# Kernel tuning notes

Hardware: AMD Instinct MI355X
Metric: run time of the kernel (lower is better)

## Reference

```python
import jax, jax.numpy as jnp
import numpy as np

N_NODES = 100000
N_EDGES = 1600000
N_GRAPHS = 64
F_IN = 256
HID = 256
PROJ = 128
L = 4


def setup_inputs() -> dict:
    key = jax.random.key(0)
    ks = jax.random.split(key, 12)
    x = jax.random.normal(ks[0], (N_NODES, F_IN), dtype=jnp.float32)
    edge_index = jax.random.randint(ks[1], (2, N_EDGES), 0, N_NODES)
    batch = jnp.sort(jax.random.randint(ks[2], (N_NODES,), 0, N_GRAPHS))
    s = 0.05
    # SAGEConv per layer: lin_l (applied to mean-aggregated neighbors, with bias)
    # and lin_r (applied to root node, no bias). All layers are 256->256, stacked.
    Wl = jax.random.normal(ks[3], (L, HID, HID), dtype=jnp.float32) * s
    bl = jax.random.normal(ks[4], (L, HID), dtype=jnp.float32) * s
    Wr = jax.random.normal(ks[5], (L, HID, HID), dtype=jnp.float32) * s
    gamma = jnp.ones((L, HID), dtype=jnp.float32)
    beta = jnp.zeros((L, HID), dtype=jnp.float32)
    W1 = jax.random.normal(ks[6], (HID, HID), dtype=jnp.float32) * s
    b1 = jnp.zeros((HID,), dtype=jnp.float32)
    W2 = jax.random.normal(ks[7], (HID, PROJ), dtype=jnp.float32) * s
    b2 = jnp.zeros((PROJ,), dtype=jnp.float32)
    return {"x": x, "edge_index": edge_index, "batch": batch,
            "Wl": Wl, "bl": bl, "Wr": Wr, "gamma": gamma, "beta": beta,
            "W1": W1, "b1": b1, "W2": W2, "b2": b2}


def _segment_mean(vals, seg_ids, num_segments):
    sums = jax.ops.segment_sum(vals, seg_ids, num_segments=num_segments)
    cnt = jax.ops.segment_sum(jnp.ones((vals.shape[0],), vals.dtype), seg_ids,
                              num_segments=num_segments)
    return sums / jnp.maximum(cnt, 1.0)[:, None]


def reference(x, edge_index, batch, Wl, bl, Wr, gamma, beta, W1, b1, W2, b2):
    src, dst = edge_index[0], edge_index[1]
    eps = 1e-5
    h = x
    for i in range(L):
        # SAGEConv: mean-aggregate neighbor features, then lin_l(aggr) + lin_r(root)
        aggr = _segment_mean(h[src], dst, N_NODES)          # [N, HID]
        h = aggr @ Wl[i] + bl[i] + h @ Wr[i]
        # BatchNorm1d (training-mode batch statistics, biased variance)
        mu = jnp.mean(h, axis=0)
        var = jnp.mean(jnp.square(h - mu), axis=0)
        h = (h - mu) * jax.lax.rsqrt(var + eps) * gamma[i] + beta[i]
        h = jax.nn.relu(h)
        # dropout omitted (inference / deterministic reference)
    g = _segment_mean(h, batch, N_GRAPHS)                   # [G, HID]
    z = jax.nn.relu(g @ W1 + b1) @ W2 + b2                  # [G, PROJ]
    # F.normalize(z, dim=1): L2 normalize with eps clamp
    norm = jnp.maximum(jnp.linalg.norm(z, axis=1, keepdims=True), 1e-12)
    return z / norm
```

## Files before the change

kernel.cpp:

```cpp
#include <hip/hip_runtime.h>

#define N_NODES 100000
#define M_PAD   100096
#define N_MBLK  782
#define N_EDGES 1600000
#define N_GRAPHS 64
#define HID 256
#define PROJ 128
#define NLAYERS 4

#define EBUF_STRIDE 8192
#define N_BUCKETS ((N_NODES + 255) / 256)
#define CSR_BLK 1024
#define EPT 10
#define CSR_NBLK ((N_EDGES + CSR_BLK * EPT - 1) / (CSR_BLK * EPT))
#define SENT 0xFFFFFFFFu
#define GEMM_BUF 24576

typedef unsigned short u16;
typedef unsigned long long u64;
typedef __attribute__((ext_vector_type(4))) float f32x4;
typedef __attribute__((ext_vector_type(2))) float vf2;

__device__ __forceinline__ u16 f2b(float f) {
  unsigned u = __float_as_uint(f);
  u = (u + 0x7FFF + ((u >> 16) & 1)) >> 16;
  return (u16)u;
}
__device__ __forceinline__ void gload16(const void* g, void* l) {
  __builtin_amdgcn_global_load_lds((const __attribute__((address_space(1))) void*)g,
                                   (__attribute__((address_space(3))) void*)l, 16, 0, 0);
}
__device__ __forceinline__ unsigned pack_fp8x4(float a, float b, float c, float d) {
  int v = __builtin_amdgcn_cvt_pk_fp8_f32(a, b, 0, false);
  v = __builtin_amdgcn_cvt_pk_fp8_f32(c, d, v, true);
  return (unsigned)v;
}
__device__ __forceinline__ unsigned char f2f8(float a) {
  return (unsigned char)(__builtin_amdgcn_cvt_pk_fp8_f32(a, a, 0, false) & 0xFF);
}
__device__ __forceinline__ void accf8(float* a, unsigned w) {
  vf2 lo = __builtin_amdgcn_cvt_pk_f32_fp8((int)w, false);
  vf2 hi = __builtin_amdgcn_cvt_pk_f32_fp8((int)w, true);
  a[0] += lo.x; a[1] += lo.y; a[2] += hi.x; a[3] += hi.y;
}
__device__ __forceinline__ void decf8(float* f, unsigned w) {
  vf2 lo = __builtin_amdgcn_cvt_pk_f32_fp8((int)w, false);
  vf2 hi = __builtin_amdgcn_cvt_pk_f32_fp8((int)w, true);
  f[0] = lo.x; f[1] = lo.y; f[2] = hi.x; f[3] = hi.y;
}

__global__ __launch_bounds__(1024) void bucket_scatter(
    const int* __restrict__ src, const int* __restrict__ dst,
    u64* __restrict__ bfill64, uint2* __restrict__ ebuf) {
  __shared__ int lhist[N_BUCKETS];
  __shared__ int lbase[N_BUCKETS];
  int t = threadIdx.x;
  int e0 = blockIdx.x * (CSR_BLK * EPT) + t;
  for (int i = t; i < N_BUCKETS; i += CSR_BLK) lhist[i] = 0;
  __syncthreads();
  int sv[EPT], dv[EPT];
#pragma unroll
  for (int j = 0; j < EPT; j++) {
    int e = e0 + j * CSR_BLK;
    if (e < N_EDGES) {
      sv[j] = src[e];
      dv[j] = dst[e];
      atomicAdd(&lhist[dv[j] >> 8], 1);
    } else {
      dv[j] = -1;
      sv[j] = 0;
    }
  }
  __syncthreads();
  for (int i = t; i < N_BUCKETS; i += CSR_BLK) {
    int c = lhist[i];
    if (c > 0) {
      int rounded = (c + 7) & ~7;
      u64 old = atomicAdd(&bfill64[(size_t)i * 8],
                          ((u64)rounded << 32) | (u64)c);
      int base = (int)(old >> 32);
      lbase[i] = base;
      for (int k = c; k < rounded; k++) {
        int p = base + k;
        if (p < EBUF_STRIDE) {
          uint2 q; q.x = 0; q.y = SENT;
          ebuf[(size_t)i * EBUF_STRIDE + p] = q;
        }
      }
      lhist[i] = 0;
    }
  }
  __syncthreads();
#pragma unroll
  for (int j = 0; j < EPT; j++) {
    if (dv[j] >= 0) {
      int b = dv[j] >> 8;
      int p = lbase[b] + atomicAdd(&lhist[b], 1);
      if (p < EBUF_STRIDE) {
        uint2 q;
        q.x = (unsigned)sv[j];
        q.y = (unsigned)dv[j];
        ebuf[(size_t)b * EBUF_STRIDE + p] = q;
      }
    }
  }
}

__global__ __launch_bounds__(512) void bucket_prefix(
    const u64* __restrict__ bfill64, int* __restrict__ bucket_base,
    int* __restrict__ row_ptr) {
  __shared__ int tile[512];
  int t = threadIdx.x;
  int v = 0;
  if (t < N_BUCKETS) {
    u64 w = bfill64[(size_t)t * 8];
    v = (int)(w & 0xFFFFFFFFull);
    if ((int)(w >> 32) > EBUF_STRIDE) v = min(v, EBUF_STRIDE);
  }
  tile[t] = v;
  __syncthreads();
  for (int off = 1; off < 512; off <<= 1) {
    int add = (t >= off) ? tile[t - off] : 0;
    __syncthreads();
    tile[t] += add;
    __syncthreads();
  }
  if (t < N_BUCKETS) bucket_base[t] = tile[t] - v;
  if (t == N_BUCKETS - 1) row_ptr[N_NODES] = tile[t];
}

__global__ __launch_bounds__(1024) void csr_build(
    const uint2* __restrict__ ebuf, const u64* __restrict__ bfill64,
    const int* __restrict__ bucket_base, int* __restrict__ row_ptr,
    float* __restrict__ inv_cnt, int* __restrict__ col) {
  __shared__ int hist[256];
  __shared__ int nscan[256];
  __shared__ int cursor[256];
  int b = blockIdx.x;
  int t = threadIdx.x;
  int nalloc = min((int)(bfill64[(size_t)b * 8] >> 32), EBUF_STRIDE);
  int bbase = bucket_base[b];
  if (t < 256) hist[t] = 0;
  __syncthreads();
  uint2 q[8];
#pragma unroll
  for (int k = 0; k < 8; k++) {
    int i = t + k * CSR_BLK;
    q[k].x = 0; q[k].y = SENT;
    if (i < nalloc) {
      q[k] = ebuf[(size_t)b * EBUF_STRIDE + i];
      if (q[k].y != SENT) atomicAdd(&hist[q[k].y & 255], 1);
    }
  }
  __syncthreads();
  if (t < 256) nscan[t] = hist[t];
  __syncthreads();
  for (int off = 1; off < 256; off <<= 1) {
    int add = 0;
    if (t < 256 && t >= off) add = nscan[t - off];
    __syncthreads();
    if (t < 256) nscan[t] += add;
    __syncthreads();
  }
  int nb = min(256, N_NODES - b * 256);
  if (t < 256) {
    int excl = nscan[t] - hist[t];
    cursor[t] = excl;
    if (t < nb) {
      row_ptr[b * 256 + t] = bbase + excl;
      inv_cnt[b * 256 + t] = 1.0f / fmaxf((float)hist[t], 1.0f);
    }
  }
  __syncthreads();
#pragma unroll
  for (int k = 0; k < 8; k++) {
    if (q[k].y != SENT) {
      int l = (int)(q[k].y & 255);
      int pos = bbase + atomicAdd(&cursor[l], 1);
      col[pos] = (int)q[k].x;
    }
  }
}

__global__ __launch_bounds__(256) void convert_x8(const float4* __restrict__ x,
                                                  unsigned* __restrict__ h8) {
  int i = blockIdx.x * blockDim.x + threadIdx.x;
  float4 v = x[i];
  h8[i] = pack_fp8x4(v.x, v.y, v.z, v.w);
}

__global__ __launch_bounds__(256) void convert_w8(const float* __restrict__ Wl,
                                                  const float* __restrict__ Wr,
                                                  unsigned* __restrict__ Wt8) {
  int idx = blockIdx.x * blockDim.x + threadIdx.x;
  int l = idx >> 15;
  int r = idx & 32767;
  int n = r >> 7;
  int k4 = (r & 127) * 4;
  float v[4];
#pragma unroll
  for (int j = 0; j < 4; j++) {
    int k = k4 + j;
    v[j] = (k < 256) ? Wl[(size_t)l * 65536 + k * 256 + n]
                     : Wr[(size_t)l * 65536 + (k - 256) * 256 + n];
  }
  Wt8[idx] = pack_fp8x4(v[0], v[1], v[2], v[3]);
}

__global__ __launch_bounds__(256) void aggregate_fp8(
    const unsigned char* __restrict__ h8, const int* __restrict__ row_ptr,
    const int* __restrict__ col, const float* __restrict__ inv_cnt,
    unsigned char* __restrict__ aggr8) {
  int node = blockIdx.x * 4 + (threadIdx.x >> 6);
  int lane = threadIdx.x & 63;
  int half = lane >> 5, l32 = lane & 31;
  int r0 = row_ptr[node], r1 = row_ptr[node + 1];
  float a[8] = {0.f, 0.f, 0.f, 0.f, 0.f, 0.f, 0.f, 0.f};
  int e = r0 + half;
  for (; e + 14 < r1; e += 16) {
    int s[8];
#pragma unroll
    for (int j = 0; j < 8; j++) s[j] = col[e + 2 * j];
    uint2 v[8];
#pragma unroll
    for (int j = 0; j < 8; j++)
      v[j] = *((const uint2*)(h8 + (size_t)s[j] * HID) + l32);
#pragma unroll
    for (int j = 0; j < 8; j++) { accf8(a, v[j].x); accf8(a + 4, v[j].y); }
  }
  for (; e + 6 < r1; e += 8) {
    int s0 = col[e], s1 = col[e + 2], s2 = col[e + 4], s3 = col[e + 6];
    uint2 v0 = *((const uint2*)(h8 + (size_t)s0 * HID) + l32);
    uint2 v1 = *((const uint2*)(h8 + (size_t)s1 * HID) + l32);
    uint2 v2 = *((const uint2*)(h8 + (size_t)s2 * HID) + l32);
    uint2 v3 = *((const uint2*)(h8 + (size_t)s3 * HID) + l32);
    accf8(a, v0.x); accf8(a + 4, v0.y);
    accf8(a, v1.x); accf8(a + 4, v1.y);
    accf8(a, v2.x); accf8(a + 4, v2.y);
    accf8(a, v3.x); accf8(a + 4, v3.y);
  }
  for (; e < r1; e += 2) {
    int s0 = col[e];
    uint2 v0 = *((const uint2*)(h8 + (size_t)s0 * HID) + l32);
    accf8(a, v0.x); accf8(a + 4, v0.y);
  }
#pragma unroll
  for (int j = 0; j < 8; j++) a[j] += __shfl_xor(a[j], 32, 64);
  if (half == 0) {
    float inv = inv_cnt[node];
    uint2 o;
    o.x = pack_fp8x4(a[0] * inv, a[1] * inv, a[2] * inv, a[3] * inv);
    o.y = pack_fp8x4(a[4] * inv, a[5] * inv, a[6] * inv, a[7] * inv);
    *((uint2*)(aggr8 + (size_t)node * HID) + l32) = o;
  }
}

__global__ __launch_bounds__(256, 2) void gemm_fused_fp8(
    const unsigned char* __restrict__ a8, const unsigned char* __restrict__ h8,
    const unsigned char* __restrict__ Bt8, unsigned char* __restrict__ hpre8,
    float* __restrict__ psum) {
  __shared__ unsigned char smem[2 * GEMM_BUF];
  __shared__ float bns[4][8][16][2];

  int tid = threadIdx.x;
  int wid = tid >> 6, lane = tid & 63;
  int m0 = blockIdx.x * 128;
  int q = lane >> 4, c = lane & 15;
  int wm = (wid >> 1) * 64, wn = (wid & 1) * 128;

  f32x4 zero = {0.f, 0.f, 0.f, 0.f};
  f32x4 acc[4][8];
#pragma unroll
  for (int mi = 0; mi < 4; mi++)
#pragma unroll
    for (int ni = 0; ni < 8; ni++) acc[mi][ni] = zero;

  int srowA0 = wid * 32 + (lane >> 2);
  int cgA0 = (lane & 3) ^ ((srowA0 >> 1) & 3);
  int srowA1 = srowA0 + 16;
  int cgA1 = (lane & 3) ^ ((srowA1 >> 1) & 3);
  int srowB[4], cgB[4];
#pragma unroll
  for (int j = 0; j < 4; j++) {
    srowB[j] = j * 64 + wid * 16 + (lane >> 2);
    cgB[j] = (lane & 3) ^ ((srowB[j] >> 1) & 3);
  }

  int aoff[4][2], boff[8][2];
#pragma unroll
  for (int mi = 0; mi < 4; mi++) {
    int row = wm + mi * 16 + c;
    int x = (row >> 1) & 3;
#pragma unroll
    for (int kk = 0; kk < 2; kk++) {
      int chunk = kk * 2 + (q >> 1);
      aoff[mi][kk] = row * 64 + ((chunk ^ x) << 4) + ((q & 1) << 3);
    }
  }
#pragma unroll
  for (int ni = 0; ni < 8; ni++) {
    int row = wn + ni * 16 + c;
    int x = (row >> 1) & 3;
#pragma unroll
    for (int kk = 0; kk < 2; kk++) {
      int chunk = kk * 2 + (q >> 1);
      boff[ni][kk] = row * 64 + ((chunk ^ x) << 4) + ((q & 1) << 3);
    }
  }

  auto stage = [&](int k0, int b) {
    const unsigned char* Asrc = (k0 < 256) ? a8 : h8;
    int ksrc = k0 & 255;
    unsigned char* As = smem + b * GEMM_BUF;
    unsigned char* Bs = As + 128 * 64;
    gload16(Asrc + ((size_t)(m0 + srowA0) * HID + ksrc + cgA0 * 16),
            &As[(wid * 32) * 64]);
    gload16(Asrc + ((size_t)(m0 + srowA1) * HID + ksrc + cgA1 * 16),
            &As[(wid * 32 + 16) * 64]);
#pragma unroll
    for (int j = 0; j < 4; j++)
      gload16(Bt8 + ((size_t)srowB[j] * 512 + k0 + cgB[j] * 16),
              &Bs[(j * 64 + wid * 16) * 64]);
  };

  stage(0, 0);
  __syncthreads();
#pragma unroll
  for (int t = 0; t < 8; ++t) {
    int cur = t & 1;
    if (t < 7) stage((t + 1) * 64, cur ^ 1);
    const unsigned char* As = smem + cur * GEMM_BUF;
    const unsigned char* Bs = As + 128 * 64;
    long long af[4][2], bfr[8][2];
#pragma unroll
    for (int mi = 0; mi < 4; mi++) {
      af[mi][0] = *(const long long*)&As[aoff[mi][0]];
      af[mi][1] = *(const long long*)&As[aoff[mi][1]];
    }
#pragma unroll
    for (int ni = 0; ni < 8; ni++) {
      bfr[ni][0] = *(const long long*)&Bs[boff[ni][0]];
      bfr[ni][1] = *(const long long*)&Bs[boff[ni][1]];
    }
#pragma unroll
    for (int mi = 0; mi < 4; mi++)
#pragma unroll
      for (int ni = 0; ni < 8; ni++) {
        acc[mi][ni] = __builtin_amdgcn_mfma_f32_16x16x32_fp8_fp8(
            af[mi][0], bfr[ni][0], acc[mi][ni], 0, 0, 0);
        acc[mi][ni] = __builtin_amdgcn_mfma_f32_16x16x32_fp8_fp8(
            af[mi][1], bfr[ni][1], acc[mi][ni], 0, 0, 0);
      }
    __syncthreads();
  }

  unsigned char* ep8 = smem;
  int rh = wid >> 1;
#pragma unroll
  for (int mi = 0; mi < 4; mi++) {
#pragma unroll
    for (int r = 0; r < 4; r++) {
      int r16 = q * 4 + r;
#pragma unroll
      for (int ni = 0; ni < 8; ni++)
        ep8[(rh * 16 + r16) * 256 + wn + ni * 16 + c] = f2f8(acc[mi][ni][r]);
    }
    __syncthreads();
    int u = tid;
#pragma unroll
    for (int j = 0; j < 2; j++, u += 256) {
      int lr = u >> 4;
      int cu = u & 15;
      int gm = m0 + (lr >> 4) * 64 + mi * 16 + (lr & 15);
      if (gm < N_NODES)
        ((uint4*)(hpre8 + (size_t)gm * HID))[cu] = ((const uint4*)ep8)[u];
    }
    __syncthreads();
  }

#pragma unroll
  for (int ni = 0; ni < 8; ni++) {
    float s = 0.f, s2 = 0.f;
#pragma unroll
    for (int mi = 0; mi < 4; mi++) {
#pragma unroll
      for (int r = 0; r < 4; r++) {
        int gm = m0 + wm + mi * 16 + q * 4 + r;
        float v = (gm < N_NODES) ? acc[mi][ni][r] : 0.f;
        s += v;
        s2 += v * v;
      }
    }
    s += __shfl_xor(s, 16, 64);
    s += __shfl_xor(s, 32, 64);
    s2 += __shfl_xor(s2, 16, 64);
    s2 += __shfl_xor(s2, 32, 64);
    if (q == 0) {
      bns[wid][ni][c][0] = s;
      bns[wid][ni][c][1] = s2;
    }
  }
  __syncthreads();
  {
    int wnh = tid >> 7, ni = (tid >> 4) & 7, cc = tid & 15;
    float s = bns[wnh][ni][cc][0] + bns[wnh + 2][ni][cc][0];
    float s2 = bns[wnh][ni][cc][1] + bns[wnh + 2][ni][cc][1];
    int coln = wnh * 128 + ni * 16 + cc;
    psum[(size_t)blockIdx.x * 512 + coln] = s;
    psum[(size_t)blockIdx.x * 512 + 256 + coln] = s2;
  }
}

#define BN_MID 16
__global__ __launch_bounds__(256) void bn_mid(const float* __restrict__ psum,
                                              float* __restrict__ tmp) {
  int b = blockIdx.x;
  int f = threadIdx.x;
  int mb0 = b * 49;
  int mb1 = min(mb0 + 49, N_MBLK);
  float s = 0.f, s2 = 0.f;
  for (int mb = mb0; mb < mb1; mb++) {
    s += psum[(size_t)mb * 512 + f];
    s2 += psum[(size_t)mb * 512 + 256 + f];
  }
  tmp[(size_t)b * 512 + f] = s;
  tmp[(size_t)b * 512 + 256 + f] = s2;
}

__global__ void bn_fin(const float* __restrict__ tmp,
                       const float* __restrict__ gamma,
                       const float* __restrict__ beta,
                       float* __restrict__ ss) {
  int f = threadIdx.x;
  float sum = 0.f, sq = 0.f;
#pragma unroll
  for (int b = 0; b < BN_MID; b++) {
    sum += tmp[(size_t)b * 512 + f];
    sq += tmp[(size_t)b * 512 + 256 + f];
  }
  const float invN = 1.0f / (float)N_NODES;
  float mu = sum * invN;
  float ex2 = sq * invN;
  float var = fmaxf(ex2 - mu * mu, 0.f);
  float sc = gamma[f] * rsqrtf(var + 1e-5f);
  ss[f] = sc;
  ss[HID + f] = beta[f] - mu * sc;
}

__global__ __launch_bounds__(256) void bn_apply_h8(const uint2* __restrict__ hpre8,
                                                   const float* __restrict__ ss,
                                                   uint2* __restrict__ h8out) {
  int idx0 = blockIdx.x * blockDim.x + threadIdx.x;
  int cb = (idx0 & 31) * 8;
  float sc[8], sh[8];
#pragma unroll
  for (int j = 0; j < 8; j++) { sc[j] = ss[cb + j]; sh[j] = ss[HID + cb + j]; }
  const int total = N_NODES * 32;
  const int step = gridDim.x * blockDim.x;
  for (int i = idx0; i < total; i += step) {
    uint2 v = hpre8[i];
    float f[8];
    decf8(f, v.x);
    decf8(f + 4, v.y);
#pragma unroll
    for (int j = 0; j < 8; j++)
      f[j] = fmaxf(fmaf(f[j], sc[j], sh[j]), 0.f);
    uint2 o;
    o.x = pack_fp8x4(f[0], f[1], f[2], f[3]);
    o.y = pack_fp8x4(f[4], f[5], f[6], f[7]);
    h8out[i] = o;
  }
}

__global__ __launch_bounds__(256) void pool_partial(
    const unsigned char* __restrict__ hpre8, const float* __restrict__ ss,
    const int* __restrict__ batch, float* __restrict__ partial) {
  __shared__ float red[256][9];
  int g = blockIdx.x;
  int i = blockIdx.y;
  int t = threadIdx.x;
  int a = 0, b = N_NODES;
  while (a < b) { int m = (a + b) >> 1; if (batch[m] < g) a = m + 1; else b = m; }
  int lo = a;
  b = N_NODES;
  while (a < b) { int m = (a + b) >> 1; if (batch[m] < g + 1) a = m + 1; else b = m; }
  int hi = a;
  int len = hi - lo;
  int clen = (len + 7) >> 3;
  int c0 = lo + i * clen;
  int c1 = min(c0 + clen, hi);

  int rs = t >> 5, cu = t & 31;
  int cb = cu * 8;
  float scv[8], shv[8];
#pragma unroll
  for (int j = 0; j < 8; j++) { scv[j] = ss[cb + j]; shv[j] = ss[HID + cb + j]; }
  float acc[8] = {0.f, 0.f, 0.f, 0.f, 0.f, 0.f, 0.f, 0.f};
  for (int r = c0 + rs; r < c1; r += 8) {
    uint2 v = *((const uint2*)(hpre8 + (size_t)r * HID) + cu);
    float f[8];
    decf8(f, v.x);
    decf8(f + 4, v.y);
#pragma unroll
    for (int j = 0; j < 8; j++)
      acc[j] += fmaxf(fmaf(f[j], scv[j], shv[j]), 0.f);
  }
#pragma unroll
  for (int j = 0; j < 8; j++) red[t][j] = acc[j];
  __syncthreads();
  int cc = t >> 3, j = t & 7;
  float sum = 0.f;
#pragma unroll
  for (int k = 0; k < 8; k++) sum += red[k * 32 + cc][j];
  partial[((size_t)g * 8 + i) * 256 + t] = sum;
}

__global__ __launch_bounds__(256) void pool_mlp_final(
    const float* __restrict__ partial, const int* __restrict__ batch,
    const float* __restrict__ W1, const float* __restrict__ b1,
    const float* __restrict__ W2, const float* __restrict__ b2,
    float* __restrict__ out) {
  __shared__ float gs[HID];
  __shared__ float ts[HID];
  __shared__ float rn[PROJ];
  int g = blockIdx.x;
  int t = threadIdx.x;
  int a = 0, b = N_NODES;
  while (a < b) { int m = (a + b) >> 1; if (batch[m] < g) a = m + 1; else b = m; }
  int lo = a;
  b = N_NODES;
  while (a < b) { int m = (a + b) >> 1; if (batch[m] < g + 1) a = m + 1; else b = m; }
  int len = a - lo;

  float sum = 0.f;
#pragma unroll
  for (int i = 0; i < 8; i++) sum += partial[((size_t)g * 8 + i) * 256 + t];
  float inv = 1.0f / fmaxf((float)len, 1.0f);
  gs[t] = sum * inv;
  __syncthreads();

  float s = b1[t];
  for (int k = 0; k < HID; k++) s = fmaf(gs[k], W1[(size_t)k * HID + t], s);
  ts[t] = fmaxf(s, 0.f);
  __syncthreads();
  float z = 0.f;
  if (t < PROJ) {
    z = b2[t];
    for (int k = 0; k < HID; k++) z = fmaf(ts[k], W2[(size_t)k * PROJ + t], z);
    rn[t] = z * z;
  }
  __syncthreads();
  for (int off = PROJ / 2; off > 0; off >>= 1) {
    if (t < off) rn[t] += rn[t + off];
    __syncthreads();
  }
  float norm = fmaxf(sqrtf(rn[0]), 1e-12f);
  if (t < PROJ) out[(size_t)g * PROJ + t] = z / norm;
}

extern "C" void kernel_launch(void* const* d_in, const int* in_sizes, int n_in,
                              void* d_out, int out_size, void* d_ws, size_t ws_size,
                              hipStream_t stream) {
  const float* x = (const float*)d_in[0];
  const int* ei = (const int*)d_in[1];
  const int* src = ei;
  const int* dst = ei + N_EDGES;
  const int* batch = (const int*)d_in[2];
  const float* Wl = (const float*)d_in[3];
  const float* Wr = (const float*)d_in[5];
  const float* gamma = (const float*)d_in[6];
  const float* beta = (const float*)d_in[7];
  const float* W1 = (const float*)d_in[8];
  const float* b1 = (const float*)d_in[9];
  const float* W2 = (const float*)d_in[10];
  const float* b2 = (const float*)d_in[11];
  float* out = (float*)d_out;

  char* p = (char*)d_ws;
  const size_t H8 = (size_t)M_PAD * HID;
  unsigned char* hpre8 = (unsigned char*)p; p += H8;
  unsigned char* aggr8 = (unsigned char*)p; p += H8;
  unsigned char* h8 = (unsigned char*)p;    p += H8;
  unsigned char* Wt8 = (unsigned char*)p;   p += (size_t)NLAYERS * 512 * HID;
  int* col = (int*)p;    p += (size_t)N_EDGES * sizeof(int);
  int* row_ptr = (int*)p; p += 400016;
  float* inv_cnt = (float*)p; p += (size_t)N_NODES * sizeof(float);
  float* psum = (float*)p;    p += (size_t)N_MBLK * 512 * sizeof(float);
  float* tmp = (float*)p;     p += (size_t)BN_MID * 512 * sizeof(float);
  float* ss = (float*)p;      p += 512 * sizeof(float);
  float* partial = (float*)p; p += (size_t)N_GRAPHS * 8 * 256 * sizeof(float);
  uint2* ebuf = (uint2*)p;    p += (size_t)N_BUCKETS * EBUF_STRIDE * sizeof(uint2);

  u64* bfill64 = (u64*)hpre8;
  int* bucket_base = (int*)(bfill64 + (size_t)N_BUCKETS * 8);

  hipMemsetAsync(bfill64, 0, (size_t)N_BUCKETS * 8 * sizeof(u64), stream);
  bucket_scatter<<<CSR_NBLK, CSR_BLK, 0, stream>>>(src, dst, bfill64, ebuf);
  bucket_prefix<<<1, 512, 0, stream>>>(bfill64, bucket_base, row_ptr);
  csr_build<<<N_BUCKETS, CSR_BLK, 0, stream>>>(ebuf, bfill64, bucket_base,
                                               row_ptr, inv_cnt, col);

  convert_x8<<<N_NODES / 4, 256, 0, stream>>>((const float4*)x, (unsigned*)h8);
  convert_w8<<<(NLAYERS * 512 * HID / 4) / 256, 256, 0, stream>>>(Wl, Wr,
                                                                  (unsigned*)Wt8);

  for (int l = 0; l < NLAYERS; l++) {
    aggregate_fp8<<<N_NODES / 4, 256, 0, stream>>>(h8, row_ptr, col, inv_cnt, aggr8);
    gemm_fused_fp8<<<N_MBLK, 256, 0, stream>>>(aggr8, h8,
                                               Wt8 + (size_t)l * 512 * HID,
                                               hpre8, psum);
    bn_mid<<<BN_MID, 256, 0, stream>>>(psum, tmp);
    bn_fin<<<1, 256, 0, stream>>>(tmp, gamma + (size_t)l * HID,
                                  beta + (size_t)l * HID, ss);
    if (l < NLAYERS - 1) {
      bn_apply_h8<<<2048, 256, 0, stream>>>((const uint2*)hpre8, ss, (uint2*)h8);
    }
  }

  pool_partial<<<dim3(N_GRAPHS, 8), 256, 0, stream>>>(hpre8, ss, batch, partial);
  pool_mlp_final<<<N_GRAPHS, 256, 0, stream>>>(partial, batch, W1, b1, W2, b2, out);
}
```

Before: 770.8 us.

## Fuse neighbor mean-aggregation into the SAGE GEMM kernel via LDS

Result: slower. 1.204 ms (+56.2%).

```diff
diff --git a/kernel.cpp b/kernel.cpp
--- a/kernel.cpp
+++ b/kernel.cpp
@@ -15,18 +15,12 @@
 #define EPT 10
 #define CSR_NBLK ((N_EDGES + CSR_BLK * EPT - 1) / (CSR_BLK * EPT))
 #define SENT 0xFFFFFFFFu
-#define GEMM_BUF 24576
 
 typedef unsigned short u16;
 typedef unsigned long long u64;
 typedef __attribute__((ext_vector_type(4))) float f32x4;
 typedef __attribute__((ext_vector_type(2))) float vf2;
 
-__device__ __forceinline__ u16 f2b(float f) {
-  unsigned u = __float_as_uint(f);
-  u = (u + 0x7FFF + ((u >> 16) & 1)) >> 16;
-  return (u16)u;
-}
 __device__ __forceinline__ void gload16(const void* g, void* l) {
   __builtin_amdgcn_global_load_lds((const __attribute__((address_space(1))) void*)g,
                                    (__attribute__((address_space(3))) void*)l, 16, 0, 0);
@@ -208,60 +202,12 @@
   Wt8[idx] = pack_fp8x4(v[0], v[1], v[2], v[3]);
 }
 
-__global__ __launch_bounds__(256) void aggregate_fp8(
+__global__ __launch_bounds__(256, 2) void agg_gemm_fused(
     const unsigned char* __restrict__ h8, const int* __restrict__ row_ptr,
     const int* __restrict__ col, const float* __restrict__ inv_cnt,
-    unsigned char* __restrict__ aggr8) {
-  int node = blockIdx.x * 4 + (threadIdx.x >> 6);
-  int lane = threadIdx.x & 63;
-  int half = lane >> 5, l32 = lane & 31;
-  int r0 = row_ptr[node], r1 = row_ptr[node + 1];
-  float a[8] = {0.f, 0.f, 0.f, 0.f, 0.f, 0.f, 0.f, 0.f};
-  int e = r0 + half;
-  for (; e + 14 < r1; e += 16) {
-    int s[8];
-#pragma unroll
-    for (int j = 0; j < 8; j++) s[j] = col[e + 2 * j];
-    uint2 v[8];
-#pragma unroll
-    for (int j = 0; j < 8; j++)
-      v[j] = *((const uint2*)(h8 + (size_t)s[j] * HID) + l32);
-#pragma unroll
-    for (int j = 0; j < 8; j++) { accf8(a, v[j].x); accf8(a + 4, v[j].y); }
-  }
-  for (; e + 6 < r1; e += 8) {
-    int s0 = col[e], s1 = col[e + 2], s2 = col[e + 4], s3 = col[e + 6];
-    uint2 v0 = *((const uint2*)(h8 + (size_t)s0 * HID) + l32);
-    uint2 v1 = *((const uint2*)(h8 + (size_t)s1 * HID) + l32);
-    uint2 v2 = *((const uint2*)(h8 + (size_t)s2 * HID) + l32);
-    uint2 v3 = *((const uint2*)(h8 + (size_t)s3 * HID) + l32);
-    accf8(a, v0.x); accf8(a + 4, v0.y);
-    accf8(a, v1.x); accf8(a + 4, v1.y);
-    accf8(a, v2.x); accf8(a + 4, v2.y);
-    accf8(a, v3.x); accf8(a + 4, v3.y);
-  }
-  for (; e < r1; e += 2) {
-    int s0 = col[e];
-    uint2 v0 = *((const uint2*)(h8 + (size_t)s0 * HID) + l32);
-    accf8(a, v0.x); accf8(a + 4, v0.y);
-  }
-#pragma unroll
-  for (int j = 0; j < 8; j++) a[j] += __shfl_xor(a[j], 32, 64);
-  if (half == 0) {
-    float inv = inv_cnt[node];
-    uint2 o;
-    o.x = pack_fp8x4(a[0] * inv, a[1] * inv, a[2] * inv, a[3] * inv);
-    o.y = pack_fp8x4(a[4] * inv, a[5] * inv, a[6] * inv, a[7] * inv);
-    *((uint2*)(aggr8 + (size_t)node * HID) + l32) = o;
-  }
-}
-
-__global__ __launch_bounds__(256, 2) void gemm_fused_fp8(
-    const unsigned char* __restrict__ a8, const unsigned char* __restrict__ h8,
     const unsigned char* __restrict__ Bt8, unsigned char* __restrict__ hpre8,
     float* __restrict__ psum) {
-  __shared__ unsigned char smem[2 * GEMM_BUF];
-  __shared__ float bns[4][8][16][2];
+  __shared__ unsigned char smem[65536];
 
   int tid = threadIdx.x;
   int wid = tid >> 6, lane = tid & 63;
@@ -309,53 +255,155 @@
     }
   }
 
-  auto stage = [&](int k0, int b) {
-    const unsigned char* Asrc = (k0 < 256) ? a8 : h8;
-    int ksrc = k0 & 255;
-    unsigned char* As = smem + b * GEMM_BUF;
-    unsigned char* Bs = As + 128 * 64;
-    gload16(Asrc + ((size_t)(m0 + srowA0) * HID + ksrc + cgA0 * 16),
-            &As[(wid * 32) * 64]);
-    gload16(Asrc + ((size_t)(m0 + srowA1) * HID + ksrc + cgA1 * 16),
-            &As[(wid * 32 + 16) * 64]);
+  {
+    auto stageA = [&](int k0, int b) {
+      unsigned char* As = smem + b * 24576;
+      unsigned char* Bs = As + 8192;
+      int ksrc = k0 - 256;
+      gload16(h8 + ((size_t)(m0 + srowA0) * HID + ksrc + cgA0 * 16),
+              &As[(wid * 32) * 64]);
+      gload16(h8 + ((size_t)(m0 + srowA1) * HID + ksrc + cgA1 * 16),
+              &As[(wid * 32 + 16) * 64]);
+#pragma unroll
+      for (int j = 0; j < 4; j++)
+        gload16(Bt8 + ((size_t)srowB[j] * 512 + k0 + cgB[j] * 16),
+                &Bs[(j * 64 + wid * 16) * 64]);
+    };
+    stageA(256, 0);
+    __syncthreads();
+#pragma unroll
+    for (int t = 0; t < 4; ++t) {
+      int cur = t & 1;
+      if (t < 3) stageA(256 + (t + 1) * 64, cur ^ 1);
+      const unsigned char* As = smem + cur * 24576;
+      const unsigned char* Bs = As + 8192;
+      long long af[4][2], bfr[8][2];
+#pragma unroll
+      for (int mi = 0; mi < 4; mi++) {
+        af[mi][0] = *(const long long*)&As[aoff[mi][0]];
+        af[mi][1] = *(const long long*)&As[aoff[mi][1]];
+      }
+#pragma unroll
+      for (int ni = 0; ni < 8; ni++) {
+        bfr[ni][0] = *(const long long*)&Bs[boff[ni][0]];
+        bfr[ni][1] = *(const long long*)&Bs[boff[ni][1]];
+      }
+#pragma unroll
+      for (int mi = 0; mi < 4; mi++)
+#pragma unroll
+        for (int ni = 0; ni < 8; ni++) {
+          acc[mi][ni] = __builtin_amdgcn_mfma_f32_16x16x32_fp8_fp8(
+              af[mi][0], bfr[ni][0], acc[mi][ni], 0, 0, 0);
+          acc[mi][ni] = __builtin_amdgcn_mfma_f32_16x16x32_fp8_fp8(
+              af[mi][1], bfr[ni][1], acc[mi][ni], 0, 0, 0);
+        }
+      __syncthreads();
+    }
+  }
+
+  {
+    unsigned char* Bs = smem + 32768;
 #pragma unroll
     for (int j = 0; j < 4; j++)
-      gload16(Bt8 + ((size_t)srowB[j] * 512 + k0 + cgB[j] * 16),
+      gload16(Bt8 + ((size_t)srowB[j] * 512 + 0 + cgB[j] * 16),
               &Bs[(j * 64 + wid * 16) * 64]);
-  };
-
-  stage(0, 0);
-  __syncthreads();
-#pragma unroll
-  for (int t = 0; t < 8; ++t) {
-    int cur = t & 1;
-    if (t < 7) stage((t + 1) * 64, cur ^ 1);
-    const unsigned char* As = smem + cur * GEMM_BUF;
-    const unsigned char* Bs = As + 128 * 64;
-    long long af[4][2], bfr[8][2];
-#pragma unroll
-    for (int mi = 0; mi < 4; mi++) {
-      af[mi][0] = *(const long long*)&As[aoff[mi][0]];
-      af[mi][1] = *(const long long*)&As[aoff[mi][1]];
-    }
-#pragma unroll
-    for (int ni = 0; ni < 8; ni++) {
-      bfr[ni][0] = *(const long long*)&Bs[boff[ni][0]];
-      bfr[ni][1] = *(const long long*)&Bs[boff[ni][1]];
-    }
-#pragma unroll
-    for (int mi = 0; mi < 4; mi++)
+  }
+
+  {
+    int half = lane >> 5, l32 = lane & 31;
+    int kstep = l32 >> 3;
+    int chunk = (l32 >> 1) & 3;
+    int bytein = (l32 & 1) * 8;
+    for (int nloc = 0; nloc < 32; ++nloc) {
+      int row = wid * 32 + nloc;
+      int node = m0 + row;
+      float a[8] = {0.f, 0.f, 0.f, 0.f, 0.f, 0.f, 0.f, 0.f};
+      bool valid = (node < N_NODES);
+      if (valid) {
+        int r0 = row_ptr[node], r1 = row_ptr[node + 1];
+        int e = r0 + half;
+        for (; e + 14 < r1; e += 16) {
+          int s[8];
+#pragma unroll
+          for (int j = 0; j < 8; j++) s[j] = col[e + 2 * j];
+          uint2 v[8];
+#pragma unroll
+          for (int j = 0; j < 8; j++)
+            v[j] = *((const uint2*)(h8 + (size_t)s[j] * HID) + l32);
+#pragma unroll
+          for (int j = 0; j < 8; j++) { accf8(a, v[j].x); accf8(a + 4, v[j].y); }
+        }
+        for (; e + 6 < r1; e += 8) {
+          int s0 = col[e], s1 = col[e + 2], s2 = col[e + 4], s3 = col[e + 6];
+          uint2 v0 = *((const uint2*)(h8 + (size_t)s0 * HID) + l32);
+          uint2 v1 = *((const uint2*)(h8 + (size_t)s1 * HID) + l32);
+          uint2 v2 = *((const uint2*)(h8 + (size_t)s2 * HID) + l32);
+          uint2 v3 = *((const uint2*)(h8 + (size_t)s3 * HID) + l32);
+          accf8(a, v0.x); accf8(a + 4, v0.y);
+          accf8(a, v1.x); accf8(a + 4, v1.y);
+          accf8(a, v2.x); accf8(a + 4, v2.y);
+          accf8(a, v3.x); accf8(a + 4, v3.y);
+        }
+        for (; e < r1; e += 2) {
+          int s0 = col[e];
+          uint2 v0 = *((const uint2*)(h8 + (size_t)s0 * HID) + l32);
+          accf8(a, v0.x); accf8(a + 4, v0.y);
+        }
+      }
+#pragma unroll
+      for (int j = 0; j < 8; j++) a[j] += __shfl_xor(a[j], 32, 64);
+      if (half == 0) {
+        float inv = valid ? inv_cnt[node] : 0.f;
+        uint2 o;
+        o.x = pack_fp8x4(a[0] * inv, a[1] * inv, a[2] * inv, a[3] * inv);
+        o.y = pack_fp8x4(a[4] * inv, a[5] * inv, a[6] * inv, a[7] * inv);
+        int chx = chunk ^ ((row >> 1) & 3);
+        *(uint2*)(smem + kstep * 8192 + row * 64 + chx * 16 + bytein) = o;
+      }
+    }
+  }
+  __syncthreads();
+
+  {
+    auto stageBC = [&](int k0, int b) {
+      unsigned char* Bs = smem + 32768 + b * 16384;
+#pragma unroll
+      for (int j = 0; j < 4; j++)
+        gload16(Bt8 + ((size_t)srowB[j] * 512 + k0 + cgB[j] * 16),
+                &Bs[(j * 64 + wid * 16) * 64]);
+    };
+#pragma unroll
+    for (int t = 0; t < 4; ++t) {
+      int cur = t & 1;
+      if (t < 3) stageBC((t + 1) * 64, cur ^ 1);
+      const unsigned char* As = smem + t * 8192;
+      const unsigned char* Bs = smem + 32768 + cur * 16384;
+      long long af[4][2], bfr[8][2];
+#pragma unroll
+      for (int mi = 0; mi < 4; mi++) {
+        af[mi][0] = *(const long long*)&As[aoff[mi][0]];
+        af[mi][1] = *(const long long*)&As[aoff[mi][1]];
+      }
 #pragma unroll
       for (int ni = 0; ni < 8; ni++) {
-        acc[mi][ni] = __builtin_amdgcn_mfma_f32_16x16x32_fp8_fp8(
-            af[mi][0], bfr[ni][0], acc[mi][ni], 0, 0, 0);
-        acc[mi][ni] = __builtin_amdgcn_mfma_f32_16x16x32_fp8_fp8(
-            af[mi][1], bfr[ni][1], acc[mi][ni], 0, 0, 0);
-      }
-    __syncthreads();
-  }
-
-  unsigned char* ep8 = smem;
+        bfr[ni][0] = *(const long long*)&Bs[boff[ni][0]];
+        bfr[ni][1] = *(const long long*)&Bs[boff[ni][1]];
+      }
+#pragma unroll
+      for (int mi = 0; mi < 4; mi++)
+#pragma unroll
+        for (int ni = 0; ni < 8; ni++) {
+          acc[mi][ni] = __builtin_amdgcn_mfma_f32_16x16x32_fp8_fp8(
+              af[mi][0], bfr[ni][0], acc[mi][ni], 0, 0, 0);
+          acc[mi][ni] = __builtin_amdgcn_mfma_f32_16x16x32_fp8_fp8(
+              af[mi][1], bfr[ni][1], acc[mi][ni], 0, 0, 0);
+        }
+      __syncthreads();
+    }
+  }
+
+  unsigned char* ep8 = smem + 32768;
+  float (*bns)[8][16][2] = (float(*)[8][16][2])(smem + 40960);
   int rh = wid >> 1;
 #pragma unroll
   for (int mi = 0; mi < 4; mi++) {
@@ -580,7 +628,6 @@
   char* p = (char*)d_ws;
   const size_t H8 = (size_t)M_PAD * HID;
   unsigned char* hpre8 = (unsigned char*)p; p += H8;
-  unsigned char* aggr8 = (unsigned char*)p; p += H8;
   unsigned char* h8 = (unsigned char*)p;    p += H8;
   unsigned char* Wt8 = (unsigned char*)p;   p += (size_t)NLAYERS * 512 * HID;
   int* col = (int*)p;    p += (size_t)N_EDGES * sizeof(int);
@@ -606,8 +653,7 @@
                                                                   (unsigned*)Wt8);
 
   for (int l = 0; l < NLAYERS; l++) {
-    aggregate_fp8<<<N_NODES / 4, 256, 0, stream>>>(h8, row_ptr, col, inv_cnt, aggr8);
-    gemm_fused_fp8<<<N_MBLK, 256, 0, stream>>>(aggr8, h8,
+    agg_gemm_fused<<<N_MBLK, 256, 0, stream>>>(h8, row_ptr, col, inv_cnt,
                                                Wt8 + (size_t)l * 512 * HID,
                                                hpre8, psum);
     bn_mid<<<BN_MID, 256, 0, stream>>>(psum, tmp);
```
